# Optimization experiments

Hardware: AMD Instinct MI355X
Metric: run time of the kernel (lower is better)

The kernel has to match this reference:

```python
import jax, jax.numpy as jnp
import numpy as np


def setup_inputs() -> dict:
    key = jax.random.key(0)
    B, C, D, H, W = 8, 2, 128, 96, 128
    corr = jax.random.normal(key, (B, C, D, H, W), dtype=jnp.float32)
    return {"corr": corr, "maxdisp": 50, "is_ux": 1}


def reference(corr, maxdisp, is_ux):
    # corr: (B, C, D, H, W). For each pixel (i, j) and displacement dx in
    # [-maxdisp, maxdisp], linearly interpolate corr along the D axis at
    # position (j + dx) if is_ux else (i + dx), with zero padding outside
    # [0, D-1] (matches grid_sample bilinear, align_corners=True, H==1).
    B, C, D, H, W = corr.shape
    K = 2 * maxdisp + 1
    dx = jnp.linspace(-float(maxdisp), float(maxdisp), K)  # (K,)
    if is_ux:
        base = jnp.broadcast_to(jnp.arange(W, dtype=jnp.float32)[None, :], (H, W))
    else:
        base = jnp.broadcast_to(jnp.arange(H, dtype=jnp.float32)[:, None], (H, W))
    pos = base[None, :, :] + dx[:, None, None]           # (K, H, W)
    i0f = jnp.floor(pos)
    w1 = (pos - i0f).astype(corr.dtype)                  # lerp weight for upper tap
    i0 = i0f.astype(jnp.int32)
    i1 = i0 + 1
    m0 = ((i0 >= 0) & (i0 < D)).astype(corr.dtype)       # zero-padding masks
    m1 = ((i1 >= 0) & (i1 < D)).astype(corr.dtype)
    idx0 = jnp.clip(i0, 0, D - 1)[None, None]            # (1,1,K,H,W) -> broadcast
    idx1 = jnp.clip(i1, 0, D - 1)[None, None]
    g0 = jnp.take_along_axis(corr, idx0, axis=2)         # (B, C, K, H, W)
    g1 = jnp.take_along_axis(corr, idx1, axis=2)
    out = g0 * ((1.0 - w1) * m0)[None, None] + g1 * (w1 * m1)[None, None]
    return out  # (B, C, 2*maxdisp+1, H, W)
```

## Files before the change

kernel.cpp:

```cpp
#include <hip/hip_runtime.h>


#define B_ 8
#define C_ 2
#define D_ 128
#define H_ 96
#define W_ 128
#define WT 64
#define NT 512
#define MAXR 114

__global__ __launch_bounds__(NT) void corr2cost_kernel(
    const float* __restrict__ corr,
    const int* __restrict__ mp,
    const int* __restrict__ up,
    float* __restrict__ out) {
  __shared__ float lds[MAXR * WT];

  const int t     = threadIdx.x;
  const int bid   = blockIdx.x;
  const int whalf = bid & 1;
  const int sl    = bid >> 1;
  const int h     = sl % H_;
  const int bc    = sl / H_;

  const int m  = *mp;
  const int ux = *up;
  const int K  = 2 * m + 1;
  const int HW = H_ * W_;
  const int w0 = whalf * WT;

  const int bmin = ux ? w0 : h;
  const int bmax = ux ? (w0 + WT - 1) : h;
  int dlo = bmin - m;        if (dlo < 0) dlo = 0;
  int dhi = bmax + K - 1 - m; if (dhi > D_ - 1) dhi = D_ - 1;
  const int R = dhi - dlo + 1;

  const float* __restrict__ src =
      corr + (size_t)bc * D_ * HW + (size_t)h * W_ + w0;
  const int nf4 = R * (WT / 4);
  for (int i = t; i < nf4; i += NT) {
    const int r  = i >> 4;
    const int c4 = (i & 15) * 4;
    *reinterpret_cast<float4*>(&lds[r * WT + c4]) =
        *reinterpret_cast<const float4*>(src + (size_t)(dlo + r) * HW + c4);
  }
  __syncthreads();

  const int w    = t & (WT - 1);
  const int kseg = t >> 6;
  const int base = ux ? (w0 + w) : h;
  float* __restrict__ dst =
      out + (size_t)bc * K * HW + (size_t)h * W_ + w0 + w;

  const int NB = (K + 7) >> 3;
  for (int kb = 0; kb < NB; kb += 7) {
    float v[7];
#pragma unroll
    for (int j = 0; j < 7; ++j) {
      const int k  = kseg + (kb + j) * 8;
      const int d  = base + k - m;
      const bool ok = (unsigned)d < (unsigned)D_;
      int rr = d - dlo;
      rr = rr < 0 ? 0 : (rr > MAXR - 1 ? MAXR - 1 : rr);
      v[j] = ok ? lds[rr * WT + w] : 0.0f;
    }
#pragma unroll
    for (int j = 0; j < 7; ++j) {
      const int k = kseg + (kb + j) * 8;
      if (k < K) dst[(size_t)k * HW] = v[j];
    }
  }
}

extern "C" void kernel_launch(void* const* d_in, const int* in_sizes, int n_in,
                              void* d_out, int out_size, void* d_ws, size_t ws_size,
                              hipStream_t stream) {
  const float* corr    = (const float*)d_in[0];
  const int*   maxdisp = (const int*)d_in[1];
  const int*   is_ux   = (const int*)d_in[2];
  float*       out     = (float*)d_out;

  const int grid = B_ * C_ * H_ * 2;
  corr2cost_kernel<<<grid, NT, 0, stream>>>(corr, maxdisp, is_ux, out);
}
```

Baseline: 173.0 us.

## Restructure to per-row-tile blocks with LDS scatter-transpose and float4 output stores

Measured after the change: 173.1 us. Within noise of the previous version (+0.1%).

```diff
diff --git a/kernel.cpp b/kernel.cpp
--- a/kernel.cpp
+++ b/kernel.cpp
@@ -6,70 +6,71 @@
 #define D_ 128
 #define H_ 96
 #define W_ 128
-#define WT 64
-#define NT 512
-#define MAXR 114
+#define TH 3
+#define NT 1024
+#define NHT (H_ / TH)
+#define NBLK (B_ * C_ * NHT)
+
+extern __shared__ float lds[];
 
 __global__ __launch_bounds__(NT) void corr2cost_kernel(
     const float* __restrict__ corr,
     const int* __restrict__ mp,
     const int* __restrict__ up,
-    float* __restrict__ out) {
-  __shared__ float lds[MAXR * WT];
+    float* __restrict__ out,
+    const int K) {
+  const int raw = blockIdx.x;
+  const int bid = (raw & 7) * (NBLK / 8) + (raw >> 3);
+  const int ht  = bid & (NHT - 1);
+  const int bc  = bid >> 5;
+  const int h0  = ht * TH;
 
-  const int t     = threadIdx.x;
-  const int bid   = blockIdx.x;
-  const int whalf = bid & 1;
-  const int sl    = bid >> 1;
-  const int h     = sl % H_;
-  const int bc    = sl / H_;
-
+  const int t  = threadIdx.x;
   const int m  = *mp;
   const int ux = *up;
-  const int K  = 2 * m + 1;
   const int HW = H_ * W_;
-  const int w0 = whalf * WT;
 
-  const int bmin = ux ? w0 : h;
-  const int bmax = ux ? (w0 + WT - 1) : h;
-  int dlo = bmin - m;        if (dlo < 0) dlo = 0;
-  int dhi = bmax + K - 1 - m; if (dhi > D_ - 1) dhi = D_ - 1;
-  const int R = dhi - dlo + 1;
-
+  const int rot = (t >> 3) & 3;
   const float* __restrict__ src =
-      corr + (size_t)bc * D_ * HW + (size_t)h * W_ + w0;
-  const int nf4 = R * (WT / 4);
-  for (int i = t; i < nf4; i += NT) {
-    const int r  = i >> 4;
-    const int c4 = (i & 15) * 4;
-    *reinterpret_cast<float4*>(&lds[r * WT + c4]) =
-        *reinterpret_cast<const float4*>(src + (size_t)(dlo + r) * HW + c4);
+      corr + (size_t)bc * D_ * HW + (size_t)h0 * W_;
+#pragma unroll
+  for (int p = 0; p < D_ * TH * (W_ / 4) / NT; ++p) {
+    const int i  = t + p * NT;
+    const int d  = i / (TH * W_ / 4);
+    const int r  = i - d * (TH * W_ / 4);
+    const int hh = r >> 5;
+    const int w4 = (r & 31) * 4;
+    const float4 v =
+        *reinterpret_cast<const float4*>(src + (size_t)d * HW + hh * W_ + w4);
+    const float vv[4] = {v.x, v.y, v.z, v.w};
+#pragma unroll
+    for (int s = 0; s < 4; ++s) {
+      const int j = (s + rot) & 3;
+      const int w = w4 + j;
+      const int k = d + m - (ux ? w : (h0 + hh));
+      if ((unsigned)k < (unsigned)K)
+        lds[(k * TH + hh) * W_ + w] = vv[j];
+    }
   }
   __syncthreads();
 
-  const int w    = t & (WT - 1);
-  const int kseg = t >> 6;
-  const int base = ux ? (w0 + w) : h;
-  float* __restrict__ dst =
-      out + (size_t)bc * K * HW + (size_t)h * W_ + w0 + w;
-
-  const int NB = (K + 7) >> 3;
-  for (int kb = 0; kb < NB; kb += 7) {
-    float v[7];
+  float* __restrict__ dst = out + (size_t)bc * K * HW + (size_t)h0 * W_;
+  const int nf4 = K * TH * (W_ / 4);
+  for (int i = t; i < nf4; i += NT) {
+    const int k  = i / (TH * W_ / 4);
+    const int r  = i - k * (TH * W_ / 4);
+    const int hh = r >> 5;
+    const int w4 = (r & 31) * 4;
+    const float4 lv =
+        *reinterpret_cast<const float4*>(&lds[(k * TH + hh) * W_ + w4]);
+    float o[4] = {lv.x, lv.y, lv.z, lv.w};
 #pragma unroll
-    for (int j = 0; j < 7; ++j) {
-      const int k  = kseg + (kb + j) * 8;
-      const int d  = base + k - m;
-      const bool ok = (unsigned)d < (unsigned)D_;
-      int rr = d - dlo;
-      rr = rr < 0 ? 0 : (rr > MAXR - 1 ? MAXR - 1 : rr);
-      v[j] = ok ? lds[rr * WT + w] : 0.0f;
+    for (int j = 0; j < 4; ++j) {
+      const int d = (ux ? (w4 + j) : (h0 + hh)) + k - m;
+      if ((unsigned)d >= (unsigned)D_) o[j] = 0.0f;
     }
-#pragma unroll
-    for (int j = 0; j < 7; ++j) {
-      const int k = kseg + (kb + j) * 8;
-      if (k < K) dst[(size_t)k * HW] = v[j];
-    }
+    *reinterpret_cast<float4*>(dst + (size_t)k * HW + hh * W_ + w4) =
+        make_float4(o[0], o[1], o[2], o[3]);
   }
 }
 
@@ -81,6 +82,9 @@
   const int*   is_ux   = (const int*)d_in[2];
   float*       out     = (float*)d_out;
 
-  const int grid = B_ * C_ * H_ * 2;
-  corr2cost_kernel<<<grid, NT, 0, stream>>>(corr, maxdisp, is_ux, out);
+  const int K = out_size / (B_ * C_ * H_ * W_);
+  const int ldsbytes = K * TH * W_ * 4;
+  hipFuncSetAttribute((const void*)corr2cost_kernel,
+                      hipFuncAttributeMaxDynamicSharedMemorySize, ldsbytes);
+  corr2cost_kernel<<<NBLK, NT, ldsbytes, stream>>>(corr, maxdisp, is_ux, out, K);
 }
```
